# Kernel tuning notes

Hardware: AMD Instinct MI355X
Metric: run time of the kernel (lower is better)

## Reference

```python
import jax, jax.numpy as jnp
import numpy as np

OUT_FEATURES = 4096
IN_FEATURES = 4096
GROUP_SIZE = 128


def setup_inputs() -> dict:
    key = jax.random.key(0)
    k1, k2, k3, k4, k5 = jax.random.split(key, 5)
    x = jax.random.normal(k1, (2, 2048, IN_FEATURES), dtype=jnp.float32)
    # Hadamard-like rotation matrix (math placeholder; orthogonality not required for correctness test)
    hadamard = jax.random.normal(k2, (IN_FEATURES, IN_FEATURES), dtype=jnp.float32) / jnp.sqrt(jnp.float32(IN_FEATURES))
    weight_scales = jax.random.uniform(k3, (OUT_FEATURES, IN_FEATURES // GROUP_SIZE), dtype=jnp.float32, minval=0.01, maxval=0.1)
    bias = jax.random.normal(k4, (OUT_FEATURES,), dtype=jnp.float32)
    # packed int4: two nibbles per byte, stored as int32 in [0, 256)
    weight_data = jax.random.randint(k5, (OUT_FEATURES, IN_FEATURES // 2), 0, 256, dtype=jnp.int32)
    return {"x": x, "hadamard": hadamard, "weight_scales": weight_scales, "bias": bias, "weight_data": weight_data}


def dequantize_int4(weight_data, weight_scales):
    # unpack nibbles: low nibble -> even K index, high nibble -> odd K index
    low = weight_data & 0xF
    high = (weight_data >> 4) & 0xF
    nibbles = jnp.stack([low, high], axis=-1).reshape(OUT_FEATURES, IN_FEATURES)  # [O, K]
    # symmetric int4: value = (nibble - 8) * group_scale
    w = (nibbles.astype(jnp.float32) - 8.0).reshape(OUT_FEATURES, IN_FEATURES // GROUP_SIZE, GROUP_SIZE)
    w = w * weight_scales[:, :, None]
    return w.reshape(OUT_FEATURES, IN_FEATURES)


def reference(x, hadamard, weight_scales, bias, weight_data):
    batch_shape = x.shape[:-1]
    x_flat = x.reshape(-1, IN_FEATURES)
    x_rot = x_flat @ hadamard  # hadamard pre-rotation
    w = dequantize_int4(weight_data, weight_scales)  # [O, K]
    out = x_rot @ w.T + bias  # [N, O]
    return out.reshape(*batch_shape, OUT_FEATURES)
```

## Files before the change

kernel.cpp:

```cpp
#include <hip/hip_runtime.h>


#define N_TOK 4096
#define K_DIM 4096
#define M_DIM 4096
#define NT    128

typedef __attribute__((ext_vector_type(8))) short s8v;
typedef __attribute__((ext_vector_type(4))) float f32x4;
typedef __attribute__((ext_vector_type(4))) unsigned short u16x4;
typedef __attribute__((ext_vector_type(8))) unsigned short u16x8;

#define AS1(p) ((const __attribute__((address_space(1))) void*)(p))
#define AS3(p) ((__attribute__((address_space(3))) void*)(p))

__device__ __forceinline__ unsigned short bf16_rne(float f) {
    unsigned int u = __float_as_uint(f);
    unsigned int r = (u + 0x7FFFu + ((u >> 16) & 1u)) >> 16;
    return (unsigned short)r;
}

__global__ __launch_bounds__(256) void prep_cast(const float* __restrict__ in,
                                                 unsigned short* __restrict__ ph) {
    size_t i = ((size_t)blockIdx.x * 256 + threadIdx.x) * 8;
    float4 v0 = *reinterpret_cast<const float4*>(&in[i]);
    float4 v1 = *reinterpret_cast<const float4*>(&in[i + 4]);
    u16x8 h;
    h[0] = bf16_rne(v0.x); h[1] = bf16_rne(v0.y);
    h[2] = bf16_rne(v0.z); h[3] = bf16_rne(v0.w);
    h[4] = bf16_rne(v1.x); h[5] = bf16_rne(v1.y);
    h[6] = bf16_rne(v1.z); h[7] = bf16_rne(v1.w);
    *reinterpret_cast<u16x8*>(&ph[i]) = h;
}

__global__ __launch_bounds__(256) void prep_hT(const float* __restrict__ H,
                                               unsigned short* __restrict__ Th) {
    __shared__ float tile[64][65];
    const int t = threadIdx.x;
    const int tx = t & 15, ty = t >> 4;
    const int c0 = blockIdx.x * 64, r0 = blockIdx.y * 64;
    #pragma unroll
    for (int rr = 0; rr < 4; ++rr) {
        int r = ty + rr * 16;
        float4 v = *reinterpret_cast<const float4*>(&H[(size_t)(r0 + r) * K_DIM + c0 + tx * 4]);
        tile[r][tx * 4 + 0] = v.x;
        tile[r][tx * 4 + 1] = v.y;
        tile[r][tx * 4 + 2] = v.z;
        tile[r][tx * 4 + 3] = v.w;
    }
    __syncthreads();
    #pragma unroll
    for (int rr = 0; rr < 4; ++rr) {
        int c = ty + rr * 16;
        u16x4 h;
        #pragma unroll
        for (int e = 0; e < 4; ++e) h[e] = bf16_rne(tile[tx * 4 + e][c]);
        size_t o = (size_t)(c0 + c) * K_DIM + r0 + tx * 4;
        *reinterpret_cast<u16x4*>(&Th[o]) = h;
    }
}

__global__ __launch_bounds__(256) void prep_w(const int* __restrict__ wd,
                                              const float* __restrict__ ws,
                                              unsigned short* __restrict__ Wb) {
    const int o = blockIdx.x, t = threadIdx.x;
    const int4* p = reinterpret_cast<const int4*>(&wd[(size_t)o * (K_DIM / 2) + t * 8]);
    int4 w0 = p[0], w1 = p[1];
    const float s = ws[o * 32 + (t >> 3)];
    int wv[8] = {w0.x, w0.y, w0.z, w0.w, w1.x, w1.y, w1.z, w1.w};
    u16x8 h0, h1;
    #pragma unroll
    for (int m = 0; m < 8; ++m) {
        unsigned short lo = bf16_rne((float)((wv[m] & 0xF) - 8) * s);
        unsigned short hi = bf16_rne((float)(((wv[m] >> 4) & 0xF) - 8) * s);
        if (m < 4) { h0[2 * m] = lo; h0[2 * m + 1] = hi; }
        else       { h1[2 * (m - 4)] = lo; h1[2 * (m - 4) + 1] = hi; }
    }
    size_t oo = (size_t)o * K_DIM + t * 16;
    *reinterpret_cast<u16x8*>(&Wb[oo]) = h0;
    *reinterpret_cast<u16x8*>(&Wb[oo + 8]) = h1;
}

template <int MODE>
__global__ __launch_bounds__(512) void gemm_cv(const unsigned short* __restrict__ A,
                                               const unsigned short* __restrict__ B,
                                               const float* __restrict__ bias,
                                               unsigned short* __restrict__ Cb,
                                               float* __restrict__ Cf) {
    extern __shared__ unsigned short sm[];
    const int t = threadIdx.x;
    const int lane = t & 63;
    const int wid = __builtin_amdgcn_readfirstlane(t >> 6);
    const int wr = wid >> 2, wc = wid & 3;

    const int fid = blockIdx.x;
    const int sw = (fid & 7) * 32 + (fid >> 3);
    const int bm = (sw >> 4) * 256;
    const int bn = (sw & 15) * 256;

    size_t ga[2], gb[2];
    int lb[2];
    #pragma unroll
    for (int j = 0; j < 2; ++j) {
        int ch = wid * 128 + j * 64 + lane;
        int row = ch >> 2, qp = ch & 3;
        int qs = qp ^ ((row >> 1) & 3);
        ga[j] = (size_t)(bm + row) * K_DIM + qs * 8;
        gb[j] = (size_t)(bn + row) * K_DIM + qs * 8;
        lb[j] = (wid * 128 + j * 64) * 8;
    }

    const int lr = lane & 15, lk = lane >> 4;
    int aoff[8], boff[4], colj[4];
    #pragma unroll
    for (int i = 0; i < 8; ++i) {
        int ra = wr * 128 + i * 16 + lr;
        aoff[i] = ra * 32 + (lk ^ ((ra >> 1) & 3)) * 8;
    }
    #pragma unroll
    for (int j = 0; j < 4; ++j) {
        int rb = wc * 64 + j * 16 + lr;
        boff[j] = rb * 32 + (lk ^ ((rb >> 1) & 3)) * 8;
        colj[j] = bn + wc * 64 + j * 16 + lr;
    }

    f32x4 acc[8][4];
    #pragma unroll
    for (int i = 0; i < 8; ++i)
        #pragma unroll
        for (int j = 0; j < 4; ++j) acc[i][j] = {0.f, 0.f, 0.f, 0.f};

#define STAGE(tt)                                                                                      \
    {                                                                                                  \
        const int _sl = ((tt) & 3) * 16384;                                                            \
        _Pragma("unroll")                                                                              \
        for (int j = 0; j < 2; ++j) {                                                                  \
            __builtin_amdgcn_global_load_lds(AS1(A + ga[j] + (tt) * 32), AS3(&sm[_sl + lb[j]]), 16, 0, 0); \
            __builtin_amdgcn_global_load_lds(AS1(B + gb[j] + (tt) * 32), AS3(&sm[_sl + 8192 + lb[j]]), 16, 0, 0); \
        }                                                                                              \
    }

#define COMPUTE(tt)                                                                                    \
    {                                                                                                  \
        const unsigned short* _pa = &sm[((tt) & 3) * 16384];                                           \
        const unsigned short* _pb = _pa + 8192;                                                        \
        s8v av[8], bv[4];                                                                              \
        _Pragma("unroll")                                                                              \
        for (int i = 0; i < 8; ++i) av[i] = *reinterpret_cast<const s8v*>(&_pa[aoff[i]]);              \
        _Pragma("unroll")                                                                              \
        for (int j = 0; j < 4; ++j) bv[j] = *reinterpret_cast<const s8v*>(&_pb[boff[j]]);              \
        _Pragma("unroll")                                                                              \
        for (int i = 0; i < 8; ++i)                                                                    \
            _Pragma("unroll")                                                                          \
            for (int j = 0; j < 4; ++j)                                                                \
                acc[i][j] = __builtin_amdgcn_mfma_f32_16x16x32_bf16(av[i], bv[j], acc[i][j], 0, 0, 0); \
    }

#define SYNCN(N)                                                                                       \
    asm volatile("s_waitcnt vmcnt(" #N ")" ::: "memory");                                              \
    __builtin_amdgcn_s_barrier();                                                                      \
    __builtin_amdgcn_sched_barrier(0);

    STAGE(0);
    STAGE(1);
    SYNCN(4);
    for (int t = 0; t + 2 < NT; ++t) {
        STAGE(t + 2);
        COMPUTE(t);
        SYNCN(4);
    }
    COMPUTE(NT - 2);
    SYNCN(0);
    COMPUTE(NT - 1);
#undef STAGE
#undef COMPUTE
#undef SYNCN

    if (MODE == 0) {
        #pragma unroll
        for (int i = 0; i < 8; ++i)
            #pragma unroll
            for (int j = 0; j < 4; ++j)
                #pragma unroll
                for (int r = 0; r < 4; ++r) {
                    int row = bm + wr * 128 + i * 16 + lk * 4 + r;
                    Cb[(size_t)row * K_DIM + colj[j]] = bf16_rne(acc[i][j][r]);
                }
    } else {
        float bj[4];
        #pragma unroll
        for (int j = 0; j < 4; ++j) bj[j] = bias[colj[j]];
        #pragma unroll
        for (int i = 0; i < 8; ++i)
            #pragma unroll
            for (int j = 0; j < 4; ++j)
                #pragma unroll
                for (int r = 0; r < 4; ++r) {
                    int row = bm + wr * 128 + i * 16 + lk * 4 + r;
                    Cf[(size_t)row * M_DIM + colj[j]] = acc[i][j][r] + bj[j];
                }
    }
}

extern "C" void kernel_launch(void* const* d_in, const int* in_sizes, int n_in,
                              void* d_out, int out_size, void* d_ws, size_t ws_size,
                              hipStream_t stream) {
    const float* x      = (const float*)d_in[0];
    const float* had    = (const float*)d_in[1];
    const float* wscale = (const float*)d_in[2];
    const float* bias   = (const float*)d_in[3];
    const int*   wdata  = (const int*)d_in[4];
    float* out = (float*)d_out;

    const size_t SEG = (size_t)N_TOK * K_DIM * 2;
    char* w = (char*)d_ws;
    unsigned short* xh  = (unsigned short*)(w);
    unsigned short* Hh  = (unsigned short*)(w + SEG);
    unsigned short* xrh = (unsigned short*)(w + 2 * SEG);
    unsigned short* Wb  = (unsigned short*)(w + 3 * SEG);

    static bool attr_done = false;
    if (!attr_done) {
        hipFuncSetAttribute((const void*)gemm_cv<0>,
                            hipFuncAttributeMaxDynamicSharedMemorySize, 131072);
        hipFuncSetAttribute((const void*)gemm_cv<1>,
                            hipFuncAttributeMaxDynamicSharedMemorySize, 131072);
        attr_done = true;
    }

    prep_cast<<<(N_TOK * K_DIM) / (256 * 8), 256, 0, stream>>>(x, xh);
    prep_hT<<<dim3(64, 64), 256, 0, stream>>>(had, Hh);
    prep_w<<<M_DIM, 256, 0, stream>>>(wdata, wscale, Wb);
    gemm_cv<0><<<256, 512, 131072, stream>>>(xh, Hh, nullptr, xrh, nullptr);
    gemm_cv<1><<<256, 512, 131072, stream>>>(xrh, Wb, bias, nullptr, out);
}
```

Baseline: 281.6 us.

## Split GEMM main loop into two phases with interleaved staging and MFMA priority

Each K-step of the GEMM main loop is split into two half-tile phases. A and B global-to-LDS staging are issued separately, each interleaved with LDS fragment reads and 16 MFMAs, and separated by extra workgroup barriers. MFMA sections are raised to a higher wave priority with s_setprio so that waves ping-pong between memory and matrix work. This adds two barriers per iteration and reorders the instruction schedule, in exchange for better overlap of loads with tensor-core work.

```diff
diff --git a/kernel.cpp b/kernel.cpp
--- a/kernel.cpp
+++ b/kernel.cpp
@@ -130,7 +130,9 @@
         #pragma unroll
         for (int j = 0; j < 4; ++j) acc[i][j] = {0.f, 0.f, 0.f, 0.f};
 
-#define STAGE(tt)                                                                                      \
+#define LD8(p) (*reinterpret_cast<const s8v*>(p))
+
+#define STAGE_AB(tt)                                                                                   \
     {                                                                                                  \
         const int _sl = ((tt) & 3) * 16384;                                                            \
         _Pragma("unroll")                                                                              \
@@ -140,15 +142,31 @@
         }                                                                                              \
     }
 
+#define STAGE_A(tt)                                                                                    \
+    {                                                                                                  \
+        const int _sl = ((tt) & 3) * 16384;                                                            \
+        _Pragma("unroll")                                                                              \
+        for (int j = 0; j < 2; ++j)                                                                    \
+            __builtin_amdgcn_global_load_lds(AS1(A + ga[j] + (tt) * 32), AS3(&sm[_sl + lb[j]]), 16, 0, 0); \
+    }
+
+#define STAGE_B(tt)                                                                                    \
+    {                                                                                                  \
+        const int _sl = ((tt) & 3) * 16384;                                                            \
+        _Pragma("unroll")                                                                              \
+        for (int j = 0; j < 2; ++j)                                                                    \
+            __builtin_amdgcn_global_load_lds(AS1(B + gb[j] + (tt) * 32), AS3(&sm[_sl + 8192 + lb[j]]), 16, 0, 0); \
+    }
+
 #define COMPUTE(tt)                                                                                    \
     {                                                                                                  \
         const unsigned short* _pa = &sm[((tt) & 3) * 16384];                                           \
         const unsigned short* _pb = _pa + 8192;                                                        \
         s8v av[8], bv[4];                                                                              \
         _Pragma("unroll")                                                                              \
-        for (int i = 0; i < 8; ++i) av[i] = *reinterpret_cast<const s8v*>(&_pa[aoff[i]]);              \
-        _Pragma("unroll")                                                                              \
-        for (int j = 0; j < 4; ++j) bv[j] = *reinterpret_cast<const s8v*>(&_pb[boff[j]]);              \
+        for (int i = 0; i < 8; ++i) av[i] = LD8(&_pa[aoff[i]]);                                        \
+        _Pragma("unroll")                                                                              \
+        for (int j = 0; j < 4; ++j) bv[j] = LD8(&_pb[boff[j]]);                                        \
         _Pragma("unroll")                                                                              \
         for (int i = 0; i < 8; ++i)                                                                    \
             _Pragma("unroll")                                                                          \
@@ -161,20 +179,54 @@
     __builtin_amdgcn_s_barrier();                                                                      \
     __builtin_amdgcn_sched_barrier(0);
 
-    STAGE(0);
-    STAGE(1);
+#define PHASE_BAR()                                                                                    \
+    __builtin_amdgcn_s_barrier();                                                                      \
+    __builtin_amdgcn_sched_barrier(0);
+
+    STAGE_AB(0);
+    STAGE_AB(1);
     SYNCN(4);
     for (int t = 0; t + 2 < NT; ++t) {
-        STAGE(t + 2);
-        COMPUTE(t);
+        const unsigned short* pa = &sm[(t & 3) * 16384];
+        const unsigned short* pb = pa + 8192;
+        s8v bv[4], a0[4], a1[4];
+        #pragma unroll
+        for (int j = 0; j < 4; ++j) bv[j] = LD8(&pb[boff[j]]);
+        #pragma unroll
+        for (int i = 0; i < 4; ++i) a0[i] = LD8(&pa[aoff[i]]);
+        STAGE_A(t + 2);
+        PHASE_BAR();
+        __builtin_amdgcn_s_setprio(1);
+        #pragma unroll
+        for (int i = 0; i < 4; ++i)
+            #pragma unroll
+            for (int j = 0; j < 4; ++j)
+                acc[i][j] = __builtin_amdgcn_mfma_f32_16x16x32_bf16(a0[i], bv[j], acc[i][j], 0, 0, 0);
+        __builtin_amdgcn_s_setprio(0);
+        PHASE_BAR();
+        #pragma unroll
+        for (int i = 0; i < 4; ++i) a1[i] = LD8(&pa[aoff[4 + i]]);
+        STAGE_B(t + 2);
+        PHASE_BAR();
+        __builtin_amdgcn_s_setprio(1);
+        #pragma unroll
+        for (int i = 0; i < 4; ++i)
+            #pragma unroll
+            for (int j = 0; j < 4; ++j)
+                acc[4 + i][j] = __builtin_amdgcn_mfma_f32_16x16x32_bf16(a1[i], bv[j], acc[4 + i][j], 0, 0, 0);
+        __builtin_amdgcn_s_setprio(0);
         SYNCN(4);
     }
     COMPUTE(NT - 2);
     SYNCN(0);
     COMPUTE(NT - 1);
-#undef STAGE
+#undef STAGE_AB
+#undef STAGE_A
+#undef STAGE_B
 #undef COMPUTE
 #undef SYNCN
+#undef PHASE_BAR
+#undef LD8
 
     if (MODE == 0) {
         #pragma unroll
```

New measurement: 284.5 us. No clear change (+1.0%).
